# Performance work log

Hardware: AMD Instinct MI355X
Metric: run time of the kernel (lower is better)

## Reference

```python
import jax, jax.numpy as jnp
import numpy as np

B, L, C = 64, 2048, 20
H1, H2, F = 384, 16, 20


def _gru(x, h0, Wih, Whh, bih, bhh):
    """PyTorch-semantics GRU, batch_first. x:(B,L,I), h0:(B,H) -> (ys:(B,L,H), hT:(B,H))."""
    H = h0.shape[-1]
    # Precompute all input projections at once: (B, L, 3H)
    xp = jnp.einsum('bli,gi->blg', x, Wih) + bih

    def step(h, xp_t):
        gh = h @ Whh.T + bhh  # (B, 3H)
        r = jax.nn.sigmoid(xp_t[:, :H] + gh[:, :H])
        z = jax.nn.sigmoid(xp_t[:, H:2 * H] + gh[:, H:2 * H])
        n = jnp.tanh(xp_t[:, 2 * H:] + r * gh[:, 2 * H:])
        h_new = (1.0 - z) * n + z * h
        return h_new, h_new

    hT, ys = jax.lax.scan(step, h0, jnp.swapaxes(xp, 0, 1))
    return jnp.swapaxes(ys, 0, 1), hT


def _init_gru(key, I, H):
    k1, k2, k3, k4 = jax.random.split(key, 4)
    s = 1.0 / np.sqrt(H)
    return (jax.random.uniform(k1, (3 * H, I), minval=-s, maxval=s),
            jax.random.uniform(k2, (3 * H, H), minval=-s, maxval=s),
            jax.random.uniform(k3, (3 * H,), minval=-s, maxval=s),
            jax.random.uniform(k4, (3 * H,), minval=-s, maxval=s))


def setup_inputs() -> dict:
    key = jax.random.key(0)
    ks = jax.random.split(key, 6)
    x = jax.random.normal(ks[0], (B, L, C), dtype=jnp.float32)
    Wih1, Whh1, bih1, bhh1 = _init_gru(ks[1], C, H1)
    Wih2, Whh2, bih2, bhh2 = _init_gru(ks[2], H1, H2)
    Wih3, Whh3, bih3, bhh3 = _init_gru(ks[3], F, F)
    s = 1.0 / np.sqrt(H2)
    Wfc = jax.random.uniform(ks[4], (F, H2), minval=-s, maxval=s)
    bfc = jax.random.uniform(ks[5], (F,), minval=-s, maxval=s)
    return {
        'x': x,
        'h1': jnp.zeros((B, H1), jnp.float32),
        'h2': jnp.zeros((B, H2), jnp.float32),
        'h3': jnp.zeros((B, F), jnp.float32),
        'Wih1': Wih1, 'Whh1': Whh1, 'bih1': bih1, 'bhh1': bhh1,
        'Wih2': Wih2, 'Whh2': Whh2, 'bih2': bih2, 'bhh2': bhh2,
        'Wih3': Wih3, 'Whh3': Whh3, 'bih3': bih3, 'bhh3': bhh3,
        'Wfc': Wfc, 'bfc': bfc,
    }


def reference(x, h1, h2, h3,
              Wih1, Whh1, bih1, bhh1,
              Wih2, Whh2, bih2, bhh2,
              Wih3, Whh3, bih3, bhh3,
              Wfc, bfc):
    y1, h1f = _gru(x, h1, Wih1, Whh1, bih1, bhh1)          # (B, L, 384)
    y2, h2f = _gru(y1, h2, Wih2, Whh2, bih2, bhh2)         # (B, L, 16)
    y2 = jax.nn.relu(y2)
    # cat of two identical copies -> dual_fc -> sum over copy dim == 2 * tanh(fc)
    x_mid = 2.0 * jnp.tanh(jnp.einsum('blh,fh->blf', y2, Wfc) + bfc)  # (B, L, 20)
    y3, h3f = _gru(jnp.flip(x_mid, axis=1), h3, Wih3, Whh3, bih3, bhh3)
    x_out = jnp.tanh(y3)                                    # (B, L, 20)
    return (x_mid, x_out, h1f, h2f, h3f)
```

## Files before the change

kernel.cpp:

```cpp
#include <hip/hip_runtime.h>

typedef _Float16 f16x8 __attribute__((ext_vector_type(8)));
typedef _Float16 f16x2 __attribute__((ext_vector_type(2)));

union F16x8U { f16x8 v8; f16x2 v2[4]; };
union FP16U { _Float16 h; unsigned short u; };

__device__ __forceinline__ float dot2acc(f16x2 a, f16x2 b, float c) {
#if __has_builtin(__builtin_amdgcn_fdot2)
    return __builtin_amdgcn_fdot2(a, b, c, false);
#else
    return c + (float)a[0] * (float)b[0] + (float)a[1] * (float)b[1];
#endif
}

__device__ __forceinline__ float sigmoidf_(float x) {
    return __builtin_amdgcn_rcpf(1.f + __expf(-x));
}

__device__ __forceinline__ float tanhf_(float x) {
    float a = fabsf(x);
    float e = __expf(-2.f * a);
    float r = (1.f - e) * __builtin_amdgcn_rcpf(1.f + e);
    return copysignf(r, x);
}


__global__ void pack_weights(const float* __restrict__ Whh1,
                             const float* __restrict__ Wih1,
                             const float* __restrict__ Wih2,
                             _Float16* __restrict__ wsbase) {
    int tid = blockIdx.x * 256 + threadIdx.x;
    f16x8* whhp  = (f16x8*)wsbase;
    f16x8* wih1p = (f16x8*)(wsbase + 442368);
    _Float16* wih2h = wsbase + 470016;
    if (tid < 55296) {
        int c = tid % 18, thr = tid / 18;
        int g = c / 6, m = c % 6;
        int jl = thr % 96, ko = (thr / 96) % 8, q = thr / 768;
        int row = g * 384 + q * 96 + jl;
        int kb = ko * 48 + m * 8;
        f16x8 v;
#pragma unroll
        for (int i = 0; i < 8; ++i) v[i] = (_Float16)Whh1[row * 384 + kb + i];
        whhp[tid] = v;
    } else if (tid < 58752) {
        int t2 = tid - 55296;
        int m = t2 % 3, thr = t2 / 3;
        int jl = thr % 96, g = (thr / 96) % 3, q = thr / 288;
        int row = g * 384 + q * 96 + jl;
        f16x8 v;
#pragma unroll
        for (int i = 0; i < 8; ++i) {
            int kk = m * 8 + i;
            v[i] = (kk < 20) ? (_Float16)Wih1[row * 20 + kk] : (_Float16)0.f;
        }
        wih1p[t2] = v;
    } else if (tid < 77184) {
        int t3 = tid - 58752;
        wih2h[t3] = (_Float16)Wih2[t3];
    }
}

__global__ __launch_bounds__(768, 3) void gru1_scan(
    const float* __restrict__ x, const float* __restrict__ h1_0,
    const float* __restrict__ bih1, const float* __restrict__ bhh1,
    const f16x8* __restrict__ whhp, const f16x8* __restrict__ wih1p,
    const _Float16* __restrict__ wih2h,
    float* __restrict__ sxp2g, unsigned* __restrict__ exch,
    float* __restrict__ h1f_o) {
    const int bid = blockIdx.x;
    const int b = bid >> 2, q = bid & 3;
    const int tid = threadIdx.x;
    const int ko = tid / 96, jl = tid % 96;
    const int lq = ko >> 1;

    __shared__ __align__(16) _Float16 h1h[384];
    __shared__ __align__(16) _Float16 hhist[4][384];
    __shared__ __align__(16) _Float16 xsh[2][24];
    __shared__ __align__(16) float4 part4[8 * 96];
    __shared__ float part2[4 * 12 * 65];

    F16x8U W[18];
    {
        const f16x8* wp = whhp + ((size_t)((q * 8 + ko) * 96 + jl)) * 18;
#pragma unroll
        for (int c = 0; c < 18; ++c) W[c].v8 = wp[c];
    }
    F16x8U Wx[3];
    if (ko < 3) {
        const f16x8* wp = wih1p + ((size_t)((q * 3 + ko) * 96 + jl)) * 3;
#pragma unroll
        for (int c = 0; c < 3; ++c) Wx[c].v8 = wp[c];
    }

    float cbr = 0.f, cbz = 0.f, cxn = 0.f, chn = 0.f, hprev = 0.f;
    if (tid < 96) {
        int j = q * 96 + tid;
        cbr = bih1[j] + bhh1[j];
        cbz = bih1[384 + j] + bhh1[384 + j];
        cxn = bih1[768 + j];
        chn = bhh1[768 + j];
        hprev = h1_0[b * 384 + j];
    }
    if (tid < 384) h1h[tid] = (_Float16)h1_0[b * 384 + tid];
    const float* xb = x + (size_t)b * 40960;
    if (tid < 24) {
        xsh[0][tid] = (_Float16)((tid < 20) ? xb[tid] : 0.f);
        xsh[1][tid] = (_Float16)0.f;
    }
    float xreg = 0.f;
    if (tid >= 96 && tid < 116) xreg = xb[20 + (tid - 96)];

    unsigned* exb0 = exch + (size_t)b * 384;
    unsigned* exb1 = exch + 24576 + (size_t)b * 384;

    const int rt = (tid < 192 * q) ? tid : tid - 192;
    const bool isloc = (lq == q);
    const int gslot = (!isloc && rt < 288) ? ((q * 96 + 96 + rt) % 384) : 0;

    const int o2 = tid >> 6, ks = tid & 63;
    const _Float16* w2row = wih2h + (q * 12 + o2) * 384 + ks * 6;

    auto gate_dots = [&](int xpar) {
        float ar = 0.f, az = 0.f, ahn = 0.f, axn = 0.f;
        const _Float16* hbase = h1h + ko * 48;
#pragma unroll
        for (int m = 0; m < 6; ++m) {
            F16x8U hv; hv.v8 = *(const f16x8*)(hbase + m * 8);
#pragma unroll
            for (int i = 0; i < 4; ++i) {
                ar  = dot2acc(W[m].v2[i],      hv.v2[i], ar);
                az  = dot2acc(W[6 + m].v2[i],  hv.v2[i], az);
                ahn = dot2acc(W[12 + m].v2[i], hv.v2[i], ahn);
            }
        }
        if (ko < 3) {
            float acc = 0.f;
            const _Float16* xs = xsh[xpar];
#pragma unroll
            for (int m = 0; m < 3; ++m) {
                F16x8U xv; xv.v8 = *(const f16x8*)(xs + m * 8);
#pragma unroll
                for (int i = 0; i < 4; ++i)
                    acc = dot2acc(Wx[m].v2[i], xv.v2[i], acc);
            }
            if (ko == 0) ar += acc;
            else if (ko == 1) az += acc;
            else axn += acc;
        }
        part4[ko * 96 + jl] = make_float4(ar, az, ahn, axn);
    };

    __syncthreads();
    gate_dots(0);
    __syncthreads();

    for (int t = 0; t < 2048; ++t) {
        const unsigned tag = (unsigned)(t + 1);
        unsigned* exw = ((t + 1) & 1) ? exb1 : exb0;

        if (tid < 96) {
            float sr = cbr, sz = cbz, snh = chn, snx = cxn;
#pragma unroll
            for (int k = 0; k < 8; ++k) {
                float4 p = part4[k * 96 + tid];
                sr += p.x; sz += p.y; snh += p.z; snx += p.w;
            }
            float r = sigmoidf_(sr), z = sigmoidf_(sz);
            float n = tanhf_(snx + r * snh);
            hprev = (1.f - z) * n + z * hprev;
            FP16U hu; hu.h = (_Float16)hprev;
            __hip_atomic_store(&exw[q * 96 + tid], (tag << 16) | (unsigned)hu.u,
                               __ATOMIC_RELAXED, __HIP_MEMORY_SCOPE_AGENT);
            h1h[q * 96 + tid] = hu.h;
            hhist[t & 3][q * 96 + tid] = hu.h;
        } else if (tid < 116) {
            xsh[(t + 1) & 1][tid - 96] = (_Float16)xreg;
            if (t + 2 < 2048) xreg = xb[(t + 2) * 20 + (tid - 96)];
        }
        __syncthreads();

        if (isloc) {
            gate_dots((t + 1) & 1);
        } else if (rt < 288) {
            unsigned w;
            do {
                w = __hip_atomic_load(&exw[gslot], __ATOMIC_RELAXED,
                                      __HIP_MEMORY_SCOPE_AGENT);
            } while ((w >> 16) != tag);
            FP16U hu; hu.u = (unsigned short)(w & 0xffffu);
            h1h[gslot] = hu.h;
            hhist[t & 3][gslot] = hu.h;
        }
        __syncthreads();

        if (!isloc) gate_dots((t + 1) & 1);

        if ((t & 3) == 3) {
            f16x2 w0 = *(const f16x2*)(w2row);
            f16x2 w1 = *(const f16x2*)(w2row + 2);
            f16x2 w2 = *(const f16x2*)(w2row + 4);
#pragma unroll
            for (int tq = 0; tq < 4; ++tq) {
                const _Float16* hrow = hhist[tq] + ks * 6;
                float a = dot2acc(w0, *(const f16x2*)hrow, 0.f);
                a = dot2acc(w1, *(const f16x2*)(hrow + 2), a);
                a = dot2acc(w2, *(const f16x2*)(hrow + 4), a);
                part2[(tq * 12 + o2) * 65 + ks] = a;
            }
            __syncthreads();
            if (tid < 48) {
                int tq = tid / 12, o = tid % 12;
                const float* pr = &part2[(tq * 12 + o) * 65];
                float s0 = 0.f, s1 = 0.f, s2 = 0.f, s3 = 0.f;
#pragma unroll
                for (int i2 = 0; i2 < 16; ++i2) {
                    s0 += pr[i2 * 4];     s1 += pr[i2 * 4 + 1];
                    s2 += pr[i2 * 4 + 2]; s3 += pr[i2 * 4 + 3];
                }
                sxp2g[((size_t)b * 2048 + (t - 3 + tq)) * 48 + q * 12 + o] =
                    (s0 + s1) + (s2 + s3);
            }
        }
        __syncthreads();
    }
    if (tid < 96) h1f_o[b * 384 + q * 96 + tid] = hprev;
}

__global__ __launch_bounds__(64) void tail_scan(
    const float* __restrict__ sxp2g, const float* __restrict__ h2_0,
    const float* __restrict__ h3_0,
    const float* __restrict__ Whh2, const float* __restrict__ bih2,
    const float* __restrict__ bhh2,
    const float* __restrict__ Wfc, const float* __restrict__ bfc,
    const float* __restrict__ Wih3, const float* __restrict__ Whh3,
    const float* __restrict__ bih3, const float* __restrict__ bhh3,
    float* __restrict__ xmid, float* __restrict__ xout,
    float* __restrict__ h2f_o, float* __restrict__ h3f_o) {
    const int b = blockIdx.x;
    const int l = threadIdx.x;

    __shared__ __align__(16) float hs[32];

    float w2r[16]; float bx2 = 0.f, bh2 = 0.f;
    if (l < 48) {
#pragma unroll
        for (int k = 0; k < 16; ++k) w2r[k] = Whh2[l * 16 + k];
        bx2 = bih2[l]; bh2 = bhh2[l];
    }
    float wfc[16]; float bf = 0.f;
    if (l < 20) {
#pragma unroll
        for (int k = 0; k < 16; ++k) wfc[k] = Wfc[l * 16 + k];
        bf = bfc[l];
    }
    float h2all[16];
    {
        const float4* hp = (const float4*)(h2_0 + b * 16);
#pragma unroll
        for (int c = 0; c < 4; ++c) {
            float4 v = hp[c];
            h2all[c * 4 + 0] = v.x; h2all[c * 4 + 1] = v.y;
            h2all[c * 4 + 2] = v.z; h2all[c * 4 + 3] = v.w;
        }
    }
    float hown = (l < 16) ? h2_0[b * 16 + l] : 0.f;

    float* xm = xmid + (size_t)b * 40960;
    const float* sx = sxp2g + (size_t)b * 98304;

    float pre[8];
#pragma unroll
    for (int i = 0; i < 8; ++i) pre[i] = (l < 48) ? sx[i * 48 + l] : 0.f;

    for (int tg = 0; tg < 256; ++tg) {
#pragma unroll
        for (int tq = 0; tq < 8; ++tq) {
            const int t = tg * 8 + tq;
            float ax = pre[tq] + bx2;
            if (l < 48 && t + 8 < 2048) pre[tq] = sx[(size_t)(t + 8) * 48 + l];
            float a0 = 0.f, a1 = 0.f;
#pragma unroll
            for (int k = 0; k < 8; ++k) {
                a0 = __builtin_fmaf(h2all[k], w2r[k], a0);
                a1 = __builtin_fmaf(h2all[8 + k], w2r[8 + k], a1);
            }
            float ah = bh2 + a0 + a1;
            float s_   = ax + ah;
            float zpre = __shfl(s_, (16 + l) & 63);
            float xn3  = __shfl(ax, (32 + l) & 63);
            float ghn  = __shfl(ah, (32 + l) & 63);
            float r2 = sigmoidf_(s_);
            float z2 = sigmoidf_(zpre);
            float n2 = tanhf_(xn3 + r2 * ghn);
            float h2n = (1.f - z2) * n2 + z2 * hown;
            if (l < 16) { hown = h2n; hs[l] = h2n; }
            __builtin_amdgcn_wave_barrier();
            {
                const float4* hv = (const float4*)hs;
#pragma unroll
                for (int c = 0; c < 4; ++c) {
                    float4 v = hv[c];
                    h2all[c * 4 + 0] = v.x; h2all[c * 4 + 1] = v.y;
                    h2all[c * 4 + 2] = v.z; h2all[c * 4 + 3] = v.w;
                }
            }
            float f0 = 0.f, f1 = 0.f;
#pragma unroll
            for (int k = 0; k < 8; ++k) {
                f0 = __builtin_fmaf(fmaxf(h2all[k], 0.f), wfc[k], f0);
                f1 = __builtin_fmaf(fmaxf(h2all[8 + k], 0.f), wfc[8 + k], f1);
            }
            float a = bf + f0 + f1;
            if (l < 20) xm[t * 20 + l] = 2.f * tanhf_(a);
        }
    }
    if (l < 16) h2f_o[b * 16 + l] = hown;

    float wi3[20], wh3[20]; float bx3 = 0.f, bh3 = 0.f;
    if (l < 60) {
#pragma unroll
        for (int k = 0; k < 20; ++k) {
            wi3[k] = Wih3[l * 20 + k];
            wh3[k] = Whh3[l * 20 + k];
        }
        bx3 = bih3[l]; bh3 = bhh3[l];
    }
    float h3all[20];
    {
        const float4* hp = (const float4*)(h3_0 + b * 20);
#pragma unroll
        for (int c = 0; c < 5; ++c) {
            float4 v = hp[c];
            h3all[c * 4 + 0] = v.x; h3all[c * 4 + 1] = v.y;
            h3all[c * 4 + 2] = v.z; h3all[c * 4 + 3] = v.w;
        }
    }
    float h3own = (l < 20) ? h3_0[b * 20 + l] : 0.f;
    float* xo = xout + (size_t)b * 40960;

    float4 px[4][5];
#pragma unroll
    for (int i = 0; i < 4; ++i) {
        const float4* xr = (const float4*)(xm + (size_t)(2047 - i) * 20);
#pragma unroll
        for (int c = 0; c < 5; ++c) px[i][c] = xr[c];
    }

    for (int tg = 0; tg < 512; ++tg) {
#pragma unroll
        for (int tq = 0; tq < 4; ++tq) {
            const int t = 2047 - (tg * 4 + tq);
            float xv[20];
#pragma unroll
            for (int c = 0; c < 5; ++c) {
                float4 v = px[tq][c];
                xv[c * 4 + 0] = v.x; xv[c * 4 + 1] = v.y;
                xv[c * 4 + 2] = v.z; xv[c * 4 + 3] = v.w;
            }
            if (t - 4 >= 0) {
                const float4* xr = (const float4*)(xm + (size_t)(t - 4) * 20);
#pragma unroll
                for (int c = 0; c < 5; ++c) px[tq][c] = xr[c];
            }
            float x0 = 0.f, x1 = 0.f, g0 = 0.f, g1 = 0.f;
#pragma unroll
            for (int k = 0; k < 10; ++k) {
                x0 = __builtin_fmaf(xv[k], wi3[k], x0);
                x1 = __builtin_fmaf(xv[10 + k], wi3[10 + k], x1);
                g0 = __builtin_fmaf(h3all[k], wh3[k], g0);
                g1 = __builtin_fmaf(h3all[10 + k], wh3[10 + k], g1);
            }
            float ax = bx3 + x0 + x1;
            float ah = bh3 + g0 + g1;
            float s_   = ax + ah;
            float zpre = __shfl(s_, (20 + l) & 63);
            float xn_  = __shfl(ax, (40 + l) & 63);
            float ghn  = __shfl(ah, (40 + l) & 63);
            float r = sigmoidf_(s_);
            float z = sigmoidf_(zpre);
            float n = tanhf_(xn_ + r * ghn);
            float hn = (1.f - z) * n + z * h3own;
            if (l < 20) {
                h3own = hn;
                hs[l] = hn;
                xo[(size_t)(2047 - t) * 20 + l] = tanhf_(hn);
            }
            __builtin_amdgcn_wave_barrier();
#pragma unroll
            for (int c = 0; c < 5; ++c) {
                float4 v = ((const float4*)hs)[c];
                h3all[c * 4 + 0] = v.x; h3all[c * 4 + 1] = v.y;
                h3all[c * 4 + 2] = v.z; h3all[c * 4 + 3] = v.w;
            }
        }
    }
    if (l < 20) h3f_o[b * 20 + l] = h3own;
}

extern "C" void kernel_launch(void* const* d_in, const int* in_sizes, int n_in,
                              void* d_out, int out_size, void* d_ws, size_t ws_size,
                              hipStream_t stream) {
    const float* x    = (const float*)d_in[0];
    const float* h1   = (const float*)d_in[1];
    const float* h2   = (const float*)d_in[2];
    const float* h3   = (const float*)d_in[3];
    const float* Wih1 = (const float*)d_in[4];
    const float* Whh1 = (const float*)d_in[5];
    const float* bih1 = (const float*)d_in[6];
    const float* bhh1 = (const float*)d_in[7];
    const float* Wih2 = (const float*)d_in[8];
    const float* Whh2 = (const float*)d_in[9];
    const float* bih2 = (const float*)d_in[10];
    const float* bhh2 = (const float*)d_in[11];
    const float* Wih3 = (const float*)d_in[12];
    const float* Whh3 = (const float*)d_in[13];
    const float* bih3 = (const float*)d_in[14];
    const float* bhh3 = (const float*)d_in[15];
    const float* Wfc  = (const float*)d_in[16];
    const float* bfc  = (const float*)d_in[17];

    float* out  = (float*)d_out;
    float* xmid = out;
    float* xout = out + 2621440;
    float* h1f  = out + 5242880;
    float* h2f  = out + 5267456;
    float* h3f  = out + 5268480;

    char* ws = (char*)d_ws;
    _Float16* wsh  = (_Float16*)ws;
    float*    sxp2 = (float*)(ws + 1048576);
    unsigned* exch = (unsigned*)(ws + 26214400);

    hipMemsetAsync(exch, 0, 196608, stream);
    pack_weights<<<302, 256, 0, stream>>>(Whh1, Wih1, Wih2, wsh);
    gru1_scan<<<256, 768, 0, stream>>>(x, h1, bih1, bhh1,
                                       (const f16x8*)wsh,
                                       (const f16x8*)(wsh + 442368),
                                       wsh + 470016,
                                       sxp2, exch, h1f);
    tail_scan<<<64, 64, 0, stream>>>(sxp2, h2, h3,
                                     Whh2, bih2, bhh2, Wfc, bfc,
                                     Wih3, Whh3, bih3, bhh3,
                                     xmid, xout, h2f, h3f);
}
```

Measured before the change: 4.997 ms.

## Overlap GRU2/FC scan with GRU1 scan via extra consumer blocks and progress flags

```diff
diff --git a/kernel.cpp b/kernel.cpp
--- a/kernel.cpp
+++ b/kernel.cpp
@@ -68,10 +68,112 @@
     const f16x8* __restrict__ whhp, const f16x8* __restrict__ wih1p,
     const _Float16* __restrict__ wih2h,
     float* __restrict__ sxp2g, unsigned* __restrict__ exch,
-    float* __restrict__ h1f_o) {
+    unsigned* __restrict__ prog, float* __restrict__ h1f_o,
+    const float* __restrict__ h2_0, const float* __restrict__ Whh2,
+    const float* __restrict__ bih2, const float* __restrict__ bhh2,
+    const float* __restrict__ Wfc, const float* __restrict__ bfc,
+    float* __restrict__ xmid, float* __restrict__ h2f_o) {
     const int bid = blockIdx.x;
+    const int tid = threadIdx.x;
+
+    if (bid >= 256) {
+        const int cb = bid - 256;
+        const int l = tid;
+        if (l >= 64) return;
+        __shared__ __align__(16) float hs2[32];
+        float w2r[16]; float bx2 = 0.f, bh2 = 0.f;
+        if (l < 48) {
+#pragma unroll
+            for (int k = 0; k < 16; ++k) w2r[k] = Whh2[l * 16 + k];
+            bx2 = bih2[l]; bh2 = bhh2[l];
+        }
+        float wfc[16]; float bf = 0.f;
+        if (l < 20) {
+#pragma unroll
+            for (int k = 0; k < 16; ++k) wfc[k] = Wfc[l * 16 + k];
+            bf = bfc[l];
+        }
+        float h2all[16];
+        {
+            const float4* hp4 = (const float4*)(h2_0 + cb * 16);
+#pragma unroll
+            for (int c = 0; c < 4; ++c) {
+                float4 v = hp4[c];
+                h2all[c * 4 + 0] = v.x; h2all[c * 4 + 1] = v.y;
+                h2all[c * 4 + 2] = v.z; h2all[c * 4 + 3] = v.w;
+            }
+        }
+        float hown = (l < 16) ? h2_0[cb * 16 + l] : 0.f;
+        float* xm = xmid + (size_t)cb * 40960;
+        const float* sx = sxp2g + (size_t)cb * 98304;
+        unsigned* pw = prog + cb * 4 + ((l < 48) ? (l / 12) : 0);
+        float pre[4] = {0.f, 0.f, 0.f, 0.f};
+        if (l < 48) {
+            while (__hip_atomic_load(pw, __ATOMIC_RELAXED,
+                                     __HIP_MEMORY_SCOPE_AGENT) < 1u)
+                __builtin_amdgcn_s_sleep(32);
+#pragma unroll
+            for (int i = 0; i < 4; ++i)
+                pre[i] = __hip_atomic_load(&sx[i * 48 + l], __ATOMIC_RELAXED,
+                                           __HIP_MEMORY_SCOPE_AGENT);
+        }
+        for (int g = 1; g <= 512; ++g) {
+#pragma unroll
+            for (int tq = 0; tq < 4; ++tq) {
+                const int t = (g - 1) * 4 + tq;
+                float ax = pre[tq] + bx2;
+                float a0 = 0.f, a1 = 0.f;
+#pragma unroll
+                for (int k = 0; k < 8; ++k) {
+                    a0 = __builtin_fmaf(h2all[k], w2r[k], a0);
+                    a1 = __builtin_fmaf(h2all[8 + k], w2r[8 + k], a1);
+                }
+                float ah = bh2 + a0 + a1;
+                float s_   = ax + ah;
+                float zpre = __shfl(s_, (16 + l) & 63);
+                float xn3  = __shfl(ax, (32 + l) & 63);
+                float ghn  = __shfl(ah, (32 + l) & 63);
+                float r2 = sigmoidf_(s_);
+                float z2 = sigmoidf_(zpre);
+                float n2 = tanhf_(xn3 + r2 * ghn);
+                float h2n = (1.f - z2) * n2 + z2 * hown;
+                if (l < 16) { hown = h2n; hs2[l] = h2n; }
+                __builtin_amdgcn_wave_barrier();
+                {
+                    const float4* hv = (const float4*)hs2;
+#pragma unroll
+                    for (int c = 0; c < 4; ++c) {
+                        float4 v = hv[c];
+                        h2all[c * 4 + 0] = v.x; h2all[c * 4 + 1] = v.y;
+                        h2all[c * 4 + 2] = v.z; h2all[c * 4 + 3] = v.w;
+                    }
+                }
+                float f0 = 0.f, f1 = 0.f;
+#pragma unroll
+                for (int k = 0; k < 8; ++k) {
+                    f0 = __builtin_fmaf(fmaxf(h2all[k], 0.f), wfc[k], f0);
+                    f1 = __builtin_fmaf(fmaxf(h2all[8 + k], 0.f), wfc[8 + k], f1);
+                }
+                float a = bf + f0 + f1;
+                if (l < 20) xm[t * 20 + l] = 2.f * tanhf_(a);
+            }
+            if (g < 512 && l < 48) {
+                while (__hip_atomic_load(pw, __ATOMIC_RELAXED,
+                                         __HIP_MEMORY_SCOPE_AGENT) <
+                       (unsigned)(g + 1))
+                    __builtin_amdgcn_s_sleep(32);
+#pragma unroll
+                for (int i = 0; i < 4; ++i)
+                    pre[i] = __hip_atomic_load(&sx[(size_t)(g * 4 + i) * 48 + l],
+                                               __ATOMIC_RELAXED,
+                                               __HIP_MEMORY_SCOPE_AGENT);
+            }
+        }
+        if (l < 16) h2f_o[cb * 16 + l] = hown;
+        return;
+    }
+
     const int b = bid >> 2, q = bid & 3;
-    const int tid = threadIdx.x;
     const int ko = tid / 96, jl = tid % 96;
     const int lq = ko >> 1;
 
@@ -159,6 +261,10 @@
     for (int t = 0; t < 2048; ++t) {
         const unsigned tag = (unsigned)(t + 1);
         unsigned* exw = ((t + 1) & 1) ? exb1 : exb0;
+
+        if ((t & 3) == 0 && t != 0 && tid == 0)
+            __hip_atomic_store(&prog[(b << 2) | q], (unsigned)(t >> 2),
+                               __ATOMIC_RELAXED, __HIP_MEMORY_SCOPE_AGENT);
 
         if (tid < 96) {
             float sr = cbr, sz = cbz, snh = chn, snx = cxn;
@@ -219,104 +325,30 @@
                     s0 += pr[i2 * 4];     s1 += pr[i2 * 4 + 1];
                     s2 += pr[i2 * 4 + 2]; s3 += pr[i2 * 4 + 3];
                 }
-                sxp2g[((size_t)b * 2048 + (t - 3 + tq)) * 48 + q * 12 + o] =
-                    (s0 + s1) + (s2 + s3);
+                __hip_atomic_store(
+                    &sxp2g[((size_t)b * 2048 + (t - 3 + tq)) * 48 + q * 12 + o],
+                    (s0 + s1) + (s2 + s3), __ATOMIC_RELAXED,
+                    __HIP_MEMORY_SCOPE_AGENT);
             }
         }
         __syncthreads();
     }
+    if (tid == 0)
+        __hip_atomic_store(&prog[(b << 2) | q], 512u,
+                           __ATOMIC_RELAXED, __HIP_MEMORY_SCOPE_AGENT);
     if (tid < 96) h1f_o[b * 384 + q * 96 + tid] = hprev;
 }
 
 __global__ __launch_bounds__(64) void tail_scan(
-    const float* __restrict__ sxp2g, const float* __restrict__ h2_0,
     const float* __restrict__ h3_0,
-    const float* __restrict__ Whh2, const float* __restrict__ bih2,
-    const float* __restrict__ bhh2,
-    const float* __restrict__ Wfc, const float* __restrict__ bfc,
     const float* __restrict__ Wih3, const float* __restrict__ Whh3,
     const float* __restrict__ bih3, const float* __restrict__ bhh3,
-    float* __restrict__ xmid, float* __restrict__ xout,
-    float* __restrict__ h2f_o, float* __restrict__ h3f_o) {
+    const float* __restrict__ xmid, float* __restrict__ xout,
+    float* __restrict__ h3f_o) {
     const int b = blockIdx.x;
     const int l = threadIdx.x;
 
     __shared__ __align__(16) float hs[32];
-
-    float w2r[16]; float bx2 = 0.f, bh2 = 0.f;
-    if (l < 48) {
-#pragma unroll
-        for (int k = 0; k < 16; ++k) w2r[k] = Whh2[l * 16 + k];
-        bx2 = bih2[l]; bh2 = bhh2[l];
-    }
-    float wfc[16]; float bf = 0.f;
-    if (l < 20) {
-#pragma unroll
-        for (int k = 0; k < 16; ++k) wfc[k] = Wfc[l * 16 + k];
-        bf = bfc[l];
-    }
-    float h2all[16];
-    {
-        const float4* hp = (const float4*)(h2_0 + b * 16);
-#pragma unroll
-        for (int c = 0; c < 4; ++c) {
-            float4 v = hp[c];
-            h2all[c * 4 + 0] = v.x; h2all[c * 4 + 1] = v.y;
-            h2all[c * 4 + 2] = v.z; h2all[c * 4 + 3] = v.w;
-        }
-    }
-    float hown = (l < 16) ? h2_0[b * 16 + l] : 0.f;
-
-    float* xm = xmid + (size_t)b * 40960;
-    const float* sx = sxp2g + (size_t)b * 98304;
-
-    float pre[8];
-#pragma unroll
-    for (int i = 0; i < 8; ++i) pre[i] = (l < 48) ? sx[i * 48 + l] : 0.f;
-
-    for (int tg = 0; tg < 256; ++tg) {
-#pragma unroll
-        for (int tq = 0; tq < 8; ++tq) {
-            const int t = tg * 8 + tq;
-            float ax = pre[tq] + bx2;
-            if (l < 48 && t + 8 < 2048) pre[tq] = sx[(size_t)(t + 8) * 48 + l];
-            float a0 = 0.f, a1 = 0.f;
-#pragma unroll
-            for (int k = 0; k < 8; ++k) {
-                a0 = __builtin_fmaf(h2all[k], w2r[k], a0);
-                a1 = __builtin_fmaf(h2all[8 + k], w2r[8 + k], a1);
-            }
-            float ah = bh2 + a0 + a1;
-            float s_   = ax + ah;
-            float zpre = __shfl(s_, (16 + l) & 63);
-            float xn3  = __shfl(ax, (32 + l) & 63);
-            float ghn  = __shfl(ah, (32 + l) & 63);
-            float r2 = sigmoidf_(s_);
-            float z2 = sigmoidf_(zpre);
-            float n2 = tanhf_(xn3 + r2 * ghn);
-            float h2n = (1.f - z2) * n2 + z2 * hown;
-            if (l < 16) { hown = h2n; hs[l] = h2n; }
-            __builtin_amdgcn_wave_barrier();
-            {
-                const float4* hv = (const float4*)hs;
-#pragma unroll
-                for (int c = 0; c < 4; ++c) {
-                    float4 v = hv[c];
-                    h2all[c * 4 + 0] = v.x; h2all[c * 4 + 1] = v.y;
-                    h2all[c * 4 + 2] = v.z; h2all[c * 4 + 3] = v.w;
-                }
-            }
-            float f0 = 0.f, f1 = 0.f;
-#pragma unroll
-            for (int k = 0; k < 8; ++k) {
-                f0 = __builtin_fmaf(fmaxf(h2all[k], 0.f), wfc[k], f0);
-                f1 = __builtin_fmaf(fmaxf(h2all[8 + k], 0.f), wfc[8 + k], f1);
-            }
-            float a = bf + f0 + f1;
-            if (l < 20) xm[t * 20 + l] = 2.f * tanhf_(a);
-        }
-    }
-    if (l < 16) h2f_o[b * 16 + l] = hown;
 
     float wi3[20], wh3[20]; float bx3 = 0.f, bh3 = 0.f;
     if (l < 60) {
@@ -338,6 +370,7 @@
         }
     }
     float h3own = (l < 20) ? h3_0[b * 20 + l] : 0.f;
+    const float* xm = xmid + (size_t)b * 40960;
     float* xo = xout + (size_t)b * 40960;
 
     float4 px[4][5];
@@ -430,18 +463,20 @@
 
     char* ws = (char*)d_ws;
     _Float16* wsh  = (_Float16*)ws;
+    unsigned* prog = (unsigned*)(ws + 1000000);
     float*    sxp2 = (float*)(ws + 1048576);
     unsigned* exch = (unsigned*)(ws + 26214400);
 
     hipMemsetAsync(exch, 0, 196608, stream);
+    hipMemsetAsync(prog, 0, 1024, stream);
     pack_weights<<<302, 256, 0, stream>>>(Whh1, Wih1, Wih2, wsh);
-    gru1_scan<<<256, 768, 0, stream>>>(x, h1, bih1, bhh1,
+    gru1_scan<<<320, 768, 0, stream>>>(x, h1, bih1, bhh1,
                                        (const f16x8*)wsh,
                                        (const f16x8*)(wsh + 442368),
                                        wsh + 470016,
-                                       sxp2, exch, h1f);
-    tail_scan<<<64, 64, 0, stream>>>(sxp2, h2, h3,
-                                     Whh2, bih2, bhh2, Wfc, bfc,
-                                     Wih3, Whh3, bih3, bhh3,
-                                     xmid, xout, h2f, h3f);
-}
+                                       sxp2, exch, prog, h1f,
+                                       h2, Whh2, bih2, bhh2, Wfc, bfc,
+                                       xmid, h2f);
+    tail_scan<<<64, 64, 0, stream>>>(h3, Wih3, Whh3, bih3, bhh3,
+                                     xmid, xout, h3f);
+}
```

After: 4.989 ms. About the same (-0.2%).
